# Kernel optimization log

Measured on AMD Instinct MI355X. Metric: run time of the kernel, lower is better.

The kernel has to match this reference:

```python
import jax, jax.numpy as jnp
import numpy as np

I, H, L, O = 11, 33, 3, 18

def lstm_layer(x_tbi, W_ih, W_hh, b_ih, b_hh):
    # x_tbi: [T, B, in]; W_ih: [4H, in]; W_hh: [4H, H]
    T, B = x_tbi.shape[0], x_tbi.shape[1]
    # precompute input contribution for all timesteps (one big GEMM)
    xg = jnp.einsum('tbi,gi->tbg', x_tbi, W_ih) + b_ih + b_hh  # [T, B, 4H]
    h0 = jnp.zeros((B, H), x_tbi.dtype)
    c0 = jnp.zeros((B, H), x_tbi.dtype)

    def step(carry, xg_t):
        h, c = carry
        gates = xg_t + h @ W_hh.T                      # [B, 4H]
        i, f, g, o = jnp.split(gates, 4, axis=-1)      # PyTorch gate order i,f,g,o
        i = jax.nn.sigmoid(i)
        f = jax.nn.sigmoid(f)
        g = jnp.tanh(g)
        o = jax.nn.sigmoid(o)
        c = f * c + i * g
        h = o * jnp.tanh(c)
        return (h, c), h

    (hT, cT), ys = jax.lax.scan(step, (h0, c0), xg)
    return ys, hT, cT  # ys: [T, B, H]


def setup_inputs() -> dict:
    key = jax.random.key(0)
    ks = jax.random.split(key, 20)
    B, T = 512, 2048
    s = 1.0 / np.sqrt(H)
    d = {'x': jax.random.normal(ks[0], (B, T, I), jnp.float32)}
    in_sizes = [I, H, H]
    for l in range(L):
        d[f'W_ih{l}'] = jax.random.uniform(ks[1 + 4 * l], (4 * H, in_sizes[l]), jnp.float32, -s, s)
        d[f'W_hh{l}'] = jax.random.uniform(ks[2 + 4 * l], (4 * H, H), jnp.float32, -s, s)
        d[f'b_ih{l}'] = jax.random.uniform(ks[3 + 4 * l], (4 * H,), jnp.float32, -s, s)
        d[f'b_hh{l}'] = jax.random.uniform(ks[4 + 4 * l], (4 * H,), jnp.float32, -s, s)
    d['W1'] = jax.random.normal(ks[13], (4 * O, H), jnp.float32) * 0.05
    d['b1'] = jnp.zeros((4 * O,), jnp.float32)
    d['W2'] = jax.random.normal(ks[14], (O, 4 * O), jnp.float32) * 0.05
    d['b2'] = jnp.zeros((O,), jnp.float32)
    return d


def reference(x, W_ih0, W_hh0, b_ih0, b_hh0, W_ih1, W_hh1, b_ih1, b_hh1,
              W_ih2, W_hh2, b_ih2, b_hh2, W1, b1, W2, b2):
    # x: [B, T, I] (batch_first) -> time-major for scan
    xt = jnp.transpose(x, (1, 0, 2))  # [T, B, I]
    params = [(W_ih0, W_hh0, b_ih0, b_hh0),
              (W_ih1, W_hh1, b_ih1, b_hh1),
              (W_ih2, W_hh2, b_ih2, b_hh2)]
    hiddens = []
    cur = xt
    for (Wi, Wh, bi, bh) in params:
        cur, hT, _ = lstm_layer(cur, Wi, Wh, bi, bh)
        hiddens.append(hT)
    hidden = jnp.stack(hiddens, axis=0)  # [L, B, H] (final hidden state per layer)
    # MLP head (dropout inactive at inference); torch nn.GELU default = exact erf
    h1 = jax.nn.gelu(hidden @ W1.T + b1, approximate=False)
    out = h1 @ W2.T + b2  # [L, B, O]
    return out, hidden
```

## Files before the change

### kernel.cpp

```cpp
#include <hip/hip_runtime.h>
#include <math.h>

#define TT 2048
#define BB 512
#define II 11
#define HH 33
#define NL 3
#define OO 18
#define HSLOT 48

typedef _Float16 h4 __attribute__((ext_vector_type(4)));
typedef _Float16 h8 __attribute__((ext_vector_type(8)));

__device__ __forceinline__ float sigm_f(float x) {
    float e = __expf(-x);
    return __builtin_amdgcn_rcpf(1.0f + e);
}
__device__ __forceinline__ float tanh_f(float x) {
    float e = __expf(2.0f * x);
    return 1.0f - 2.0f * __builtin_amdgcn_rcpf(e + 1.0f);
}

__device__ __forceinline__ float dpp_xor1(float v) {
    return __builtin_bit_cast(float,
        __builtin_amdgcn_update_dpp(0, __builtin_bit_cast(int, v), 0xB1, 0xF, 0xF, true));
}

__device__ __forceinline__ h8 gldh8(const float* p, int k0, int rem) {
    h8 v;
    #pragma unroll
    for (int i = 0; i < 8; ++i) v[i] = (_Float16)((k0 + i < rem) ? p[k0 + i] : 0.0f);
    return v;
}
__device__ __forceinline__ h4 gldh4(const float* p, int k0, int rem) {
    h4 v;
    #pragma unroll
    for (int i = 0; i < 4; ++i) v[i] = (_Float16)((k0 + i < rem) ? p[k0 + i] : 0.0f);
    return v;
}

#define D8(a, v, w) do { \
    a = __builtin_amdgcn_fdot2((v).s01, (w).s01, a, false); \
    a = __builtin_amdgcn_fdot2((v).s23, (w).s23, a, false); \
    a = __builtin_amdgcn_fdot2((v).s45, (w).s45, a, false); \
    a = __builtin_amdgcn_fdot2((v).s67, (w).s67, a, false); } while (0)
#define D4(a, v, w) do { \
    a = __builtin_amdgcn_fdot2((v).s01, (w).s01, a, false); \
    a = __builtin_amdgcn_fdot2((v).s23, (w).s23, a, false); } while (0)

__global__ __launch_bounds__(256, 2) void lstm_pipeline_kernel(
    const float* __restrict__ x,
    const float* __restrict__ Wih0, const float* __restrict__ Whh0,
    const float* __restrict__ bih0, const float* __restrict__ bhh0,
    const float* __restrict__ Wih1, const float* __restrict__ Whh1,
    const float* __restrict__ bih1, const float* __restrict__ bhh1,
    const float* __restrict__ Wih2, const float* __restrict__ Whh2,
    const float* __restrict__ bih2, const float* __restrict__ bhh2,
    float* __restrict__ hidden_out)
{
    __shared__ __align__(16) _Float16 buf[2][NL + 1][HSLOT];

    const int tid = threadIdx.x;
    const int bg  = blockIdx.x;

    for (int i = tid; i < 2 * (NL + 1) * HSLOT; i += 256)
        ((_Float16*)buf)[i] = (_Float16)0.0f;

    const bool comp = (tid < 198);
    const int  u    = tid >> 1;
    const int  p    = tid & 1;
    const int  l    = (u < 33) ? 0 : (u < 66) ? 1 : 2;
    const int  j    = u - 33 * l;

    const int  pi   = tid - 198;
    const bool pref = (pi >= 0) && (pi < II);
    const float* xrow = x + (size_t)bg * TT * II + (pref ? pi : 0);

    h8 z8 = {0,0,0,0,0,0,0,0};
    h4 z4 = {0,0,0,0};
    h8 w0a=z8,w0b=z8,w0c=z8,w0d=z8; h4 w0t=z4;
    h8 w1a=z8,w1b=z8,w1c=z8,w1d=z8; h4 w1t=z4;
    h8 w2a=z8,w2b=z8,w2c=z8,w2d=z8; h4 w2t=z4;
    h8 w3a=z8,w3b=z8,w3c=z8,w3d=z8; h4 w3t=z4;
    float b0 = 0.0f, b1 = 0.0f, b2 = 0.0f, b3 = 0.0f;

    if (comp) {
        const float* bip = (l == 0) ? bih0 : (l == 1) ? bih1 : bih2;
        const float* bhp = (l == 0) ? bhh0 : (l == 1) ? bhh1 : bhh2;
        if (p == 0) {
            b0 = bip[0 * HH + j] + bhp[0 * HH + j];
            b1 = bip[1 * HH + j] + bhp[1 * HH + j];
            b2 = bip[2 * HH + j] + bhp[2 * HH + j];
            b3 = bip[3 * HH + j] + bhp[3 * HH + j];
        }
        const float* Wsrc = p ? ((l == 0) ? Whh0 : (l == 1) ? Whh1 : Whh2)
                              : ((l == 0) ? Wih0 : (l == 1) ? Wih1 : Wih2);
        const int kin = (p || l != 0) ? HH : II;
        const float* r0 = Wsrc + (0 * HH + j) * kin;
        const float* r1 = Wsrc + (1 * HH + j) * kin;
        const float* r2 = Wsrc + (2 * HH + j) * kin;
        const float* r3 = Wsrc + (3 * HH + j) * kin;
        w0a = gldh8(r0, 0, kin); w0b = gldh8(r0, 8, kin);
        w0c = gldh8(r0, 16, kin); w0d = gldh8(r0, 24, kin); w0t = gldh4(r0, 32, kin);
        w1a = gldh8(r1, 0, kin); w1b = gldh8(r1, 8, kin);
        w1c = gldh8(r1, 16, kin); w1d = gldh8(r1, 24, kin); w1t = gldh4(r1, 32, kin);
        w2a = gldh8(r2, 0, kin); w2b = gldh8(r2, 8, kin);
        w2c = gldh8(r2, 16, kin); w2d = gldh8(r2, 24, kin); w2t = gldh4(r2, 32, kin);
        w3a = gldh8(r3, 0, kin); w3b = gldh8(r3, 8, kin);
        w3c = gldh8(r3, 16, kin); w3d = gldh8(r3, 24, kin); w3t = gldh4(r3, 32, kin);
    }

    __syncthreads();
    float v_next = 0.0f, v_next2 = 0.0f;
    if (pref) {
        buf[0][0][pi] = (_Float16)xrow[0];
        v_next  = xrow[II];
        v_next2 = xrow[2 * II];
    }
    __syncthreads();

    float c = 0.0f;
    const int   vsel = p ? (l + 1) : l;
    const float mA   = 1.0f + (float)p;
    const float cAc  = -(float)p;
    const bool  wrh  = comp && (p == 0);

    const _Float16* rd[2]  = { &buf[0][vsel][0], &buf[1][vsel][0] };
    _Float16*       wrp[2] = { &buf[0][l + 1][j], &buf[1][l + 1][j] };
    _Float16*       pxp[2] = { &buf[0][0][pi], &buf[1][0][pi] };

    auto step = [&](int s, int rp, bool check, bool out, bool xload, bool xstore)
        __attribute__((always_inline)) {
        const int wp = rp ^ 1;
        if (pref) {
            if (xstore) *pxp[wp] = (_Float16)v_next;
            v_next = v_next2;
            if (xload) v_next2 = xrow[(size_t)(s + 3) * II];
        }
        const bool active = check ? (comp && (s >= l) && (s - l < TT)) : comp;
        if (active) {
            const _Float16* V16 = rd[rp];
            const h8* V = (const h8*)V16;
            const h8 v0 = V[0], v1 = V[1], v2 = V[2], v3 = V[3];
            const h4 vt = *(const h4*)(V16 + 32);

            float a0 = b0, a1 = b1, a2 = b2, a3 = b3;
            D8(a0, v0, w0a); D8(a1, v0, w1a); D8(a2, v0, w2a); D8(a3, v0, w3a);
            D8(a0, v1, w0b); D8(a1, v1, w1b); D8(a2, v1, w2b); D8(a3, v1, w3b);
            D8(a0, v2, w0c); D8(a1, v2, w1c); D8(a2, v2, w2c); D8(a3, v2, w3c);
            D8(a0, v3, w0d); D8(a1, v3, w1d); D8(a2, v3, w2d); D8(a3, v3, w3d);
            D4(a0, vt, w0t); D4(a1, vt, w1t); D4(a2, vt, w2t); D4(a3, vt, w3t);

            a0 += dpp_xor1(a0); a1 += dpp_xor1(a1);
            a2 += dpp_xor1(a2); a3 += dpp_xor1(a3);

            const float aA = p ? a2 : a0;
            const float aB = p ? a3 : a1;
            const float acta = __builtin_fmaf(mA, sigm_f(mA * aA), cAc);
            const float actb = sigm_f(aB);
            const float xa = dpp_xor1(acta);
            const float xb = dpp_xor1(actb);
            const float ig = p ? xa : acta;
            const float gg = p ? acta : xa;
            const float fg = p ? xb : actb;
            const float og = p ? actb : xb;

            c = __builtin_fmaf(fg, c, ig * gg);
            const float hnew = og * tanh_f(c);

            if (wrh) {
                *wrp[wp] = (_Float16)hnew;
                if (out && (s - l == TT - 1))
                    hidden_out[((size_t)l * BB + bg) * HH + j] = hnew;
            }
        }
        __syncthreads();
    };

    step(0, 0, true, false, true, true);
    step(1, 1, true, false, true, true);
    for (int s = 2; s < TT - 4; s += 2) {
        step(s,     0, false, false, true, true);
        step(s + 1, 1, false, false, true, true);
    }
    step(TT - 4, 0, false, false, true,  true);
    step(TT - 3, 1, false, false, false, true);
    step(TT - 2, 0, false, false, false, true);
    step(TT - 1, 1, false, true,  false, false);
    step(TT,     0, true,  true,  false, false);
    step(TT + 1, 1, true,  true,  false, false);
}

__global__ void mlp_head_kernel(const float* __restrict__ hidden,
                                const float* __restrict__ W1, const float* __restrict__ b1,
                                const float* __restrict__ W2, const float* __restrict__ b2,
                                float* __restrict__ out)
{
    const int row = blockIdx.x * blockDim.x + threadIdx.x;
    if (row >= NL * BB) return;

    float hv[HH];
    #pragma unroll
    for (int k = 0; k < HH; ++k) hv[k] = hidden[row * HH + k];

    float h1[4 * OO];
    #pragma unroll
    for (int m = 0; m < 4 * OO; ++m) {
        float a = b1[m];
        #pragma unroll
        for (int k = 0; k < HH; ++k) a += hv[k] * W1[m * HH + k];
        h1[m] = 0.5f * a * (1.0f + erff(a * 0.70710678118654752f));
    }
    #pragma unroll
    for (int o = 0; o < OO; ++o) {
        float a = b2[o];
        #pragma unroll
        for (int m = 0; m < 4 * OO; ++m) a += h1[m] * W2[o * (4 * OO) + m];
        out[row * OO + o] = a;
    }
}

extern "C" void kernel_launch(void* const* d_in, const int* in_sizes, int n_in,
                              void* d_out, int out_size, void* d_ws, size_t ws_size,
                              hipStream_t stream) {
    const float* x    = (const float*)d_in[0];
    const float* Wih0 = (const float*)d_in[1];
    const float* Whh0 = (const float*)d_in[2];
    const float* bih0 = (const float*)d_in[3];
    const float* bhh0 = (const float*)d_in[4];
    const float* Wih1 = (const float*)d_in[5];
    const float* Whh1 = (const float*)d_in[6];
    const float* bih1 = (const float*)d_in[7];
    const float* bhh1 = (const float*)d_in[8];
    const float* Wih2 = (const float*)d_in[9];
    const float* Whh2 = (const float*)d_in[10];
    const float* bih2 = (const float*)d_in[11];
    const float* bhh2 = (const float*)d_in[12];
    const float* W1   = (const float*)d_in[13];
    const float* b1   = (const float*)d_in[14];
    const float* W2   = (const float*)d_in[15];
    const float* b2   = (const float*)d_in[16];

    float* out    = (float*)d_out;
    float* hidden = out + NL * BB * OO;

    lstm_pipeline_kernel<<<BB, 256, 0, stream>>>(
        x, Wih0, Whh0, bih0, bhh0, Wih1, Whh1, bih1, bhh1,
        Wih2, Whh2, bih2, bhh2, hidden);

    mlp_head_kernel<<<(NL * BB + 255) / 256, 256, 0, stream>>>(
        hidden, W1, b1, W2, b2, out);
}
```

Before: 1.190 ms.

## Use packed fp16 FMA accumulation for gate dot products and fuse MLP head

Replaces the fp32-accumulating fdot2 chains with packed half-precision FMAs into two h2 accumulators per gate, reduced across lanes in fp16 and then converted to fp32 with the bias. This halves the dependent chain length and uses packed math to shorten the per-timestep recurrent critical path. It also folds the MLP head into the LSTM kernel's epilogue using shared memory, removing a second launch. Accumulating 33-term dot products in fp16 reduces accuracy and may breach tolerance over 2048 recurrent steps.

Result: slower. 1.249 ms (+4.9%).

```diff
diff --git a/kernel.cpp b/kernel.cpp
--- a/kernel.cpp
+++ b/kernel.cpp
@@ -9,6 +9,7 @@
 #define OO 18
 #define HSLOT 48
 
+typedef _Float16 h2 __attribute__((ext_vector_type(2)));
 typedef _Float16 h4 __attribute__((ext_vector_type(4)));
 typedef _Float16 h8 __attribute__((ext_vector_type(8)));
 
@@ -23,6 +24,10 @@
 
 __device__ __forceinline__ float dpp_xor1(float v) {
     return __builtin_bit_cast(float,
+        __builtin_amdgcn_update_dpp(0, __builtin_bit_cast(int, v), 0xB1, 0xF, 0xF, true));
+}
+__device__ __forceinline__ h2 dpp_xor1_h2(h2 v) {
+    return __builtin_bit_cast(h2,
         __builtin_amdgcn_update_dpp(0, __builtin_bit_cast(int, v), 0xB1, 0xF, 0xF, true));
 }
 
@@ -39,14 +44,12 @@
     return v;
 }
 
-#define D8(a, v, w) do { \
-    a = __builtin_amdgcn_fdot2((v).s01, (w).s01, a, false); \
-    a = __builtin_amdgcn_fdot2((v).s23, (w).s23, a, false); \
-    a = __builtin_amdgcn_fdot2((v).s45, (w).s45, a, false); \
-    a = __builtin_amdgcn_fdot2((v).s67, (w).s67, a, false); } while (0)
-#define D4(a, v, w) do { \
-    a = __builtin_amdgcn_fdot2((v).s01, (w).s01, a, false); \
-    a = __builtin_amdgcn_fdot2((v).s23, (w).s23, a, false); } while (0)
+#define PF(acc, vv, ww) acc = __builtin_elementwise_fma((vv), (ww), (acc))
+#define PK8(A, B, v, w) do { \
+    PF(A, (v).s01, (w).s01); PF(B, (v).s23, (w).s23); \
+    PF(A, (v).s45, (w).s45); PF(B, (v).s67, (w).s67); } while (0)
+#define PK4(A, B, v, w) do { \
+    PF(A, (v).s01, (w).s01); PF(B, (v).s23, (w).s23); } while (0)
 
 __global__ __launch_bounds__(256, 2) void lstm_pipeline_kernel(
     const float* __restrict__ x,
@@ -56,9 +59,14 @@
     const float* __restrict__ bih1, const float* __restrict__ bhh1,
     const float* __restrict__ Wih2, const float* __restrict__ Whh2,
     const float* __restrict__ bih2, const float* __restrict__ bhh2,
-    float* __restrict__ hidden_out)
+    const float* __restrict__ W1, const float* __restrict__ b1,
+    const float* __restrict__ W2, const float* __restrict__ b2,
+    float* __restrict__ hidden_out,
+    float* __restrict__ outp)
 {
     __shared__ __align__(16) _Float16 buf[2][NL + 1][HSLOT];
+    __shared__ float hfin[NL][HH];
+    __shared__ float h1s[NL][4 * OO];
 
     const int tid = threadIdx.x;
     const int bg  = blockIdx.x;
@@ -82,17 +90,16 @@
     h8 w1a=z8,w1b=z8,w1c=z8,w1d=z8; h4 w1t=z4;
     h8 w2a=z8,w2b=z8,w2c=z8,w2d=z8; h4 w2t=z4;
     h8 w3a=z8,w3b=z8,w3c=z8,w3d=z8; h4 w3t=z4;
-    float b0 = 0.0f, b1 = 0.0f, b2 = 0.0f, b3 = 0.0f;
+    float b0 = 0.0f, b1v = 0.0f, b2v = 0.0f, b3v = 0.0f;
 
     if (comp) {
         const float* bip = (l == 0) ? bih0 : (l == 1) ? bih1 : bih2;
         const float* bhp = (l == 0) ? bhh0 : (l == 1) ? bhh1 : bhh2;
-        if (p == 0) {
-            b0 = bip[0 * HH + j] + bhp[0 * HH + j];
-            b1 = bip[1 * HH + j] + bhp[1 * HH + j];
-            b2 = bip[2 * HH + j] + bhp[2 * HH + j];
-            b3 = bip[3 * HH + j] + bhp[3 * HH + j];
-        }
+        b0  = bip[0 * HH + j] + bhp[0 * HH + j];
+        b1v = bip[1 * HH + j] + bhp[1 * HH + j];
+        b2v = bip[2 * HH + j] + bhp[2 * HH + j];
+        b3v = bip[3 * HH + j] + bhp[3 * HH + j];
+
         const float* Wsrc = p ? ((l == 0) ? Whh0 : (l == 1) ? Whh1 : Whh2)
                               : ((l == 0) ? Wih0 : (l == 1) ? Wih1 : Wih2);
         const int kin = (p || l != 0) ? HH : II;
@@ -144,15 +151,28 @@
             const h8 v0 = V[0], v1 = V[1], v2 = V[2], v3 = V[3];
             const h4 vt = *(const h4*)(V16 + 32);
 
-            float a0 = b0, a1 = b1, a2 = b2, a3 = b3;
-            D8(a0, v0, w0a); D8(a1, v0, w1a); D8(a2, v0, w2a); D8(a3, v0, w3a);
-            D8(a0, v1, w0b); D8(a1, v1, w1b); D8(a2, v1, w2b); D8(a3, v1, w3b);
-            D8(a0, v2, w0c); D8(a1, v2, w1c); D8(a2, v2, w2c); D8(a3, v2, w3c);
-            D8(a0, v3, w0d); D8(a1, v3, w1d); D8(a2, v3, w2d); D8(a3, v3, w3d);
-            D4(a0, vt, w0t); D4(a1, vt, w1t); D4(a2, vt, w2t); D4(a3, vt, w3t);
-
-            a0 += dpp_xor1(a0); a1 += dpp_xor1(a1);
-            a2 += dpp_xor1(a2); a3 += dpp_xor1(a3);
+            h2 z2 = {(_Float16)0.0f, (_Float16)0.0f};
+            h2 A0 = z2, B0 = z2, A1 = z2, B1 = z2;
+            h2 A2 = z2, B2 = z2, A3 = z2, B3 = z2;
+            PK8(A0, B0, v0, w0a); PK8(A1, B1, v0, w1a);
+            PK8(A2, B2, v0, w2a); PK8(A3, B3, v0, w3a);
+            PK8(A0, B0, v1, w0b); PK8(A1, B1, v1, w1b);
+            PK8(A2, B2, v1, w2b); PK8(A3, B3, v1, w3b);
+            PK8(A0, B0, v2, w0c); PK8(A1, B1, v2, w1c);
+            PK8(A2, B2, v2, w2c); PK8(A3, B3, v2, w3c);
+            PK8(A0, B0, v3, w0d); PK8(A1, B1, v3, w1d);
+            PK8(A2, B2, v3, w2d); PK8(A3, B3, v3, w3d);
+            PK4(A0, B0, vt, w0t); PK4(A1, B1, vt, w1t);
+            PK4(A2, B2, vt, w2t); PK4(A3, B3, vt, w3t);
+
+            h2 t0 = A0 + B0, t1 = A1 + B1, t2 = A2 + B2, t3 = A3 + B3;
+            t0 += dpp_xor1_h2(t0); t1 += dpp_xor1_h2(t1);
+            t2 += dpp_xor1_h2(t2); t3 += dpp_xor1_h2(t3);
+
+            const float a0 = b0  + ((float)t0.x + (float)t0.y);
+            const float a1 = b1v + ((float)t1.x + (float)t1.y);
+            const float a2 = b2v + ((float)t2.x + (float)t2.y);
+            const float a3 = b3v + ((float)t3.x + (float)t3.y);
 
             const float aA = p ? a2 : a0;
             const float aB = p ? a3 : a1;
@@ -170,8 +190,10 @@
 
             if (wrh) {
                 *wrp[wp] = (_Float16)hnew;
-                if (out && (s - l == TT - 1))
+                if (out && (s - l == TT - 1)) {
                     hidden_out[((size_t)l * BB + bg) * HH + j] = hnew;
+                    hfin[l][j] = hnew;
+                }
             }
         }
         __syncthreads();
@@ -189,34 +211,21 @@
     step(TT - 1, 1, false, true,  false, false);
     step(TT,     0, true,  true,  false, false);
     step(TT + 1, 1, true,  true,  false, false);
-}
-
-__global__ void mlp_head_kernel(const float* __restrict__ hidden,
-                                const float* __restrict__ W1, const float* __restrict__ b1,
-                                const float* __restrict__ W2, const float* __restrict__ b2,
-                                float* __restrict__ out)
-{
-    const int row = blockIdx.x * blockDim.x + threadIdx.x;
-    if (row >= NL * BB) return;
-
-    float hv[HH];
-    #pragma unroll
-    for (int k = 0; k < HH; ++k) hv[k] = hidden[row * HH + k];
-
-    float h1[4 * OO];
-    #pragma unroll
-    for (int m = 0; m < 4 * OO; ++m) {
+
+    if (tid < NL * 4 * OO) {
+        const int ml = tid / (4 * OO), m = tid % (4 * OO);
         float a = b1[m];
         #pragma unroll
-        for (int k = 0; k < HH; ++k) a += hv[k] * W1[m * HH + k];
-        h1[m] = 0.5f * a * (1.0f + erff(a * 0.70710678118654752f));
-    }
-    #pragma unroll
-    for (int o = 0; o < OO; ++o) {
+        for (int k = 0; k < HH; ++k) a += hfin[ml][k] * W1[m * HH + k];
+        h1s[ml][m] = 0.5f * a * (1.0f + erff(a * 0.70710678118654752f));
+    }
+    __syncthreads();
+    if (tid < NL * OO) {
+        const int ol = tid / OO, o = tid % OO;
         float a = b2[o];
         #pragma unroll
-        for (int m = 0; m < 4 * OO; ++m) a += h1[m] * W2[o * (4 * OO) + m];
-        out[row * OO + o] = a;
+        for (int m = 0; m < 4 * OO; ++m) a += h1s[ol][m] * W2[o * (4 * OO) + m];
+        outp[((size_t)ol * BB + bg) * OO + o] = a;
     }
 }
 
@@ -246,8 +255,5 @@
 
     lstm_pipeline_kernel<<<BB, 256, 0, stream>>>(
         x, Wih0, Whh0, bih0, bhh0, Wih1, Whh1, bih1, bhh1,
-        Wih2, Whh2, bih2, bhh2, hidden);
-
-    mlp_head_kernel<<<(NL * BB + 255) / 256, 256, 0, stream>>>(
-        hidden, W1, b1, W2, b2, out);
-}
+        Wih2, Whh2, bih2, bhh2, W1, b1, W2, b2, hidden, out);
+}
```

## Use one thread per hidden unit instead of paired threads per unit

Applied to the files above, without the earlier changes.

Each hidden unit is now computed by a single thread that holds both the input and recurrent weight rows in registers. This removes the DPP cross-lane reductions and gate exchanges, and shrinks the block from 256 to 128 threads (two waves instead of four), which cuts barrier cost. The price is twice the serial dot-product work per thread on the recurrent critical path and roughly double the weight registers per thread. It also drops the padded tail from 4 to 2 halves.

After: 1.150 ms. 3.4% less time.

```diff
diff --git a/kernel.cpp b/kernel.cpp
--- a/kernel.cpp
+++ b/kernel.cpp
@@ -9,7 +9,7 @@
 #define OO 18
 #define HSLOT 48
 
-typedef _Float16 h4 __attribute__((ext_vector_type(4)));
+typedef _Float16 h2 __attribute__((ext_vector_type(2)));
 typedef _Float16 h8 __attribute__((ext_vector_type(8)));
 
 __device__ __forceinline__ float sigm_f(float x) {
@@ -21,21 +21,16 @@
     return 1.0f - 2.0f * __builtin_amdgcn_rcpf(e + 1.0f);
 }
 
-__device__ __forceinline__ float dpp_xor1(float v) {
-    return __builtin_bit_cast(float,
-        __builtin_amdgcn_update_dpp(0, __builtin_bit_cast(int, v), 0xB1, 0xF, 0xF, true));
-}
-
 __device__ __forceinline__ h8 gldh8(const float* p, int k0, int rem) {
     h8 v;
     #pragma unroll
     for (int i = 0; i < 8; ++i) v[i] = (_Float16)((k0 + i < rem) ? p[k0 + i] : 0.0f);
     return v;
 }
-__device__ __forceinline__ h4 gldh4(const float* p, int k0, int rem) {
-    h4 v;
-    #pragma unroll
-    for (int i = 0; i < 4; ++i) v[i] = (_Float16)((k0 + i < rem) ? p[k0 + i] : 0.0f);
+__device__ __forceinline__ h2 gldh2(const float* p, int k0, int rem) {
+    h2 v;
+    v.x = (_Float16)((k0 + 0 < rem) ? p[k0 + 0] : 0.0f);
+    v.y = (_Float16)((k0 + 1 < rem) ? p[k0 + 1] : 0.0f);
     return v;
 }
 
@@ -44,11 +39,9 @@
     a = __builtin_amdgcn_fdot2((v).s23, (w).s23, a, false); \
     a = __builtin_amdgcn_fdot2((v).s45, (w).s45, a, false); \
     a = __builtin_amdgcn_fdot2((v).s67, (w).s67, a, false); } while (0)
-#define D4(a, v, w) do { \
-    a = __builtin_amdgcn_fdot2((v).s01, (w).s01, a, false); \
-    a = __builtin_amdgcn_fdot2((v).s23, (w).s23, a, false); } while (0)
-
-__global__ __launch_bounds__(256, 2) void lstm_pipeline_kernel(
+#define D1(a, v, w) a = __builtin_amdgcn_fdot2((v), (w), a, false)
+
+__global__ __launch_bounds__(128, 1) void lstm_pipeline_kernel(
     const float* __restrict__ x,
     const float* __restrict__ Wih0, const float* __restrict__ Whh0,
     const float* __restrict__ bih0, const float* __restrict__ bhh0,
@@ -63,51 +56,57 @@
     const int tid = threadIdx.x;
     const int bg  = blockIdx.x;
 
-    for (int i = tid; i < 2 * (NL + 1) * HSLOT; i += 256)
+    for (int i = tid; i < 2 * (NL + 1) * HSLOT; i += 128)
         ((_Float16*)buf)[i] = (_Float16)0.0f;
 
-    const bool comp = (tid < 198);
-    const int  u    = tid >> 1;
-    const int  p    = tid & 1;
+    const bool comp = (tid < 99);
+    const int  u    = tid;
     const int  l    = (u < 33) ? 0 : (u < 66) ? 1 : 2;
     const int  j    = u - 33 * l;
 
-    const int  pi   = tid - 198;
+    const int  pi   = tid - 99;
     const bool pref = (pi >= 0) && (pi < II);
     const float* xrow = x + (size_t)bg * TT * II + (pref ? pi : 0);
 
     h8 z8 = {0,0,0,0,0,0,0,0};
-    h4 z4 = {0,0,0,0};
-    h8 w0a=z8,w0b=z8,w0c=z8,w0d=z8; h4 w0t=z4;
-    h8 w1a=z8,w1b=z8,w1c=z8,w1d=z8; h4 w1t=z4;
-    h8 w2a=z8,w2b=z8,w2c=z8,w2d=z8; h4 w2t=z4;
-    h8 w3a=z8,w3b=z8,w3c=z8,w3d=z8; h4 w3t=z4;
+    h2 z2 = {(_Float16)0.0f, (_Float16)0.0f};
+    h8 x00=z8,x01=z8,x02=z8,x03=z8; h2 x0t=z2;
+    h8 x10=z8,x11=z8,x12=z8,x13=z8; h2 x1t=z2;
+    h8 x20=z8,x21=z8,x22=z8,x23=z8; h2 x2t=z2;
+    h8 x30=z8,x31=z8,x32=z8,x33=z8; h2 x3t=z2;
+    h8 h00=z8,h01=z8,h02=z8,h03=z8; h2 h0t=z2;
+    h8 h10=z8,h11=z8,h12=z8,h13=z8; h2 h1t=z2;
+    h8 h20=z8,h21=z8,h22=z8,h23=z8; h2 h2t=z2;
+    h8 h30=z8,h31=z8,h32=z8,h33=z8; h2 h3t=z2;
     float b0 = 0.0f, b1 = 0.0f, b2 = 0.0f, b3 = 0.0f;
 
     if (comp) {
         const float* bip = (l == 0) ? bih0 : (l == 1) ? bih1 : bih2;
         const float* bhp = (l == 0) ? bhh0 : (l == 1) ? bhh1 : bhh2;
-        if (p == 0) {
-            b0 = bip[0 * HH + j] + bhp[0 * HH + j];
-            b1 = bip[1 * HH + j] + bhp[1 * HH + j];
-            b2 = bip[2 * HH + j] + bhp[2 * HH + j];
-            b3 = bip[3 * HH + j] + bhp[3 * HH + j];
-        }
-        const float* Wsrc = p ? ((l == 0) ? Whh0 : (l == 1) ? Whh1 : Whh2)
-                              : ((l == 0) ? Wih0 : (l == 1) ? Wih1 : Wih2);
-        const int kin = (p || l != 0) ? HH : II;
-        const float* r0 = Wsrc + (0 * HH + j) * kin;
-        const float* r1 = Wsrc + (1 * HH + j) * kin;
-        const float* r2 = Wsrc + (2 * HH + j) * kin;
-        const float* r3 = Wsrc + (3 * HH + j) * kin;
-        w0a = gldh8(r0, 0, kin); w0b = gldh8(r0, 8, kin);
-        w0c = gldh8(r0, 16, kin); w0d = gldh8(r0, 24, kin); w0t = gldh4(r0, 32, kin);
-        w1a = gldh8(r1, 0, kin); w1b = gldh8(r1, 8, kin);
-        w1c = gldh8(r1, 16, kin); w1d = gldh8(r1, 24, kin); w1t = gldh4(r1, 32, kin);
-        w2a = gldh8(r2, 0, kin); w2b = gldh8(r2, 8, kin);
-        w2c = gldh8(r2, 16, kin); w2d = gldh8(r2, 24, kin); w2t = gldh4(r2, 32, kin);
-        w3a = gldh8(r3, 0, kin); w3b = gldh8(r3, 8, kin);
-        w3c = gldh8(r3, 16, kin); w3d = gldh8(r3, 24, kin); w3t = gldh4(r3, 32, kin);
+        b0 = bip[0 * HH + j] + bhp[0 * HH + j];
+        b1 = bip[1 * HH + j] + bhp[1 * HH + j];
+        b2 = bip[2 * HH + j] + bhp[2 * HH + j];
+        b3 = bip[3 * HH + j] + bhp[3 * HH + j];
+
+        const float* Wi = (l == 0) ? Wih0 : (l == 1) ? Wih1 : Wih2;
+        const float* Wh = (l == 0) ? Whh0 : (l == 1) ? Whh1 : Whh2;
+        const int kin = (l == 0) ? II : HH;
+        const float* r0 = Wi + (0 * HH + j) * kin;
+        const float* r1 = Wi + (1 * HH + j) * kin;
+        const float* r2 = Wi + (2 * HH + j) * kin;
+        const float* r3 = Wi + (3 * HH + j) * kin;
+        x00=gldh8(r0,0,kin); x01=gldh8(r0,8,kin); x02=gldh8(r0,16,kin); x03=gldh8(r0,24,kin); x0t=gldh2(r0,32,kin);
+        x10=gldh8(r1,0,kin); x11=gldh8(r1,8,kin); x12=gldh8(r1,16,kin); x13=gldh8(r1,24,kin); x1t=gldh2(r1,32,kin);
+        x20=gldh8(r2,0,kin); x21=gldh8(r2,8,kin); x22=gldh8(r2,16,kin); x23=gldh8(r2,24,kin); x2t=gldh2(r2,32,kin);
+        x30=gldh8(r3,0,kin); x31=gldh8(r3,8,kin); x32=gldh8(r3,16,kin); x33=gldh8(r3,24,kin); x3t=gldh2(r3,32,kin);
+        const float* s0 = Wh + (0 * HH + j) * HH;
+        const float* s1 = Wh + (1 * HH + j) * HH;
+        const float* s2 = Wh + (2 * HH + j) * HH;
+        const float* s3 = Wh + (3 * HH + j) * HH;
+        h00=gldh8(s0,0,HH); h01=gldh8(s0,8,HH); h02=gldh8(s0,16,HH); h03=gldh8(s0,24,HH); h0t=gldh2(s0,32,HH);
+        h10=gldh8(s1,0,HH); h11=gldh8(s1,8,HH); h12=gldh8(s1,16,HH); h13=gldh8(s1,24,HH); h1t=gldh2(s1,32,HH);
+        h20=gldh8(s2,0,HH); h21=gldh8(s2,8,HH); h22=gldh8(s2,16,HH); h23=gldh8(s2,24,HH); h2t=gldh2(s2,32,HH);
+        h30=gldh8(s3,0,HH); h31=gldh8(s3,8,HH); h32=gldh8(s3,16,HH); h33=gldh8(s3,24,HH); h3t=gldh2(s3,32,HH);
     }
 
     __syncthreads();
@@ -120,14 +119,11 @@
     __syncthreads();
 
     float c = 0.0f;
-    const int   vsel = p ? (l + 1) : l;
-    const float mA   = 1.0f + (float)p;
-    const float cAc  = -(float)p;
-    const bool  wrh  = comp && (p == 0);
-
-    const _Float16* rd[2]  = { &buf[0][vsel][0], &buf[1][vsel][0] };
-    _Float16*       wrp[2] = { &buf[0][l + 1][j], &buf[1][l + 1][j] };
-    _Float16*       pxp[2] = { &buf[0][0][pi], &buf[1][0][pi] };
+
+    const _Float16* rin[2]  = { &buf[0][l][0],     &buf[1][l][0] };
+    const _Float16* rown[2] = { &buf[0][l + 1][0], &buf[1][l + 1][0] };
+    _Float16*       wrp[2]  = { &buf[0][l + 1][j], &buf[1][l + 1][j] };
+    _Float16*       pxp[2]  = { &buf[0][0][pi],    &buf[1][0][pi] };
 
     auto step = [&](int s, int rp, bool check, bool out, bool xload, bool xstore)
         __attribute__((always_inline)) {
@@ -139,40 +135,35 @@
         }
         const bool active = check ? (comp && (s >= l) && (s - l < TT)) : comp;
         if (active) {
-            const _Float16* V16 = rd[rp];
-            const h8* V = (const h8*)V16;
-            const h8 v0 = V[0], v1 = V[1], v2 = V[2], v3 = V[3];
-            const h4 vt = *(const h4*)(V16 + 32);
+            const h8* VI = (const h8*)rin[rp];
+            const h8 vi0 = VI[0], vi1 = VI[1], vi2 = VI[2], vi3 = VI[3];
+            const h2 vit = *(const h2*)(rin[rp] + 32);
+            const h8* VO = (const h8*)rown[rp];
+            const h8 vo0 = VO[0], vo1 = VO[1], vo2 = VO[2], vo3 = VO[3];
+            const h2 vot = *(const h2*)(rown[rp] + 32);
 
             float a0 = b0, a1 = b1, a2 = b2, a3 = b3;
-            D8(a0, v0, w0a); D8(a1, v0, w1a); D8(a2, v0, w2a); D8(a3, v0, w3a);
-            D8(a0, v1, w0b); D8(a1, v1, w1b); D8(a2, v1, w2b); D8(a3, v1, w3b);
-            D8(a0, v2, w0c); D8(a1, v2, w1c); D8(a2, v2, w2c); D8(a3, v2, w3c);
-            D8(a0, v3, w0d); D8(a1, v3, w1d); D8(a2, v3, w2d); D8(a3, v3, w3d);
-            D4(a0, vt, w0t); D4(a1, vt, w1t); D4(a2, vt, w2t); D4(a3, vt, w3t);
-
-            a0 += dpp_xor1(a0); a1 += dpp_xor1(a1);
-            a2 += dpp_xor1(a2); a3 += dpp_xor1(a3);
-
-            const float aA = p ? a2 : a0;
-            const float aB = p ? a3 : a1;
-            const float acta = __builtin_fmaf(mA, sigm_f(mA * aA), cAc);
-            const float actb = sigm_f(aB);
-            const float xa = dpp_xor1(acta);
-            const float xb = dpp_xor1(actb);
-            const float ig = p ? xa : acta;
-            const float gg = p ? acta : xa;
-            const float fg = p ? xb : actb;
-            const float og = p ? actb : xb;
-
+            D8(a0, vi0, x00); D8(a1, vi0, x10); D8(a2, vi0, x20); D8(a3, vi0, x30);
+            D8(a0, vi1, x01); D8(a1, vi1, x11); D8(a2, vi1, x21); D8(a3, vi1, x31);
+            D8(a0, vi2, x02); D8(a1, vi2, x12); D8(a2, vi2, x22); D8(a3, vi2, x32);
+            D8(a0, vi3, x03); D8(a1, vi3, x13); D8(a2, vi3, x23); D8(a3, vi3, x33);
+            D1(a0, vit, x0t); D1(a1, vit, x1t); D1(a2, vit, x2t); D1(a3, vit, x3t);
+            D8(a0, vo0, h00); D8(a1, vo0, h10); D8(a2, vo0, h20); D8(a3, vo0, h30);
+            D8(a0, vo1, h01); D8(a1, vo1, h11); D8(a2, vo1, h21); D8(a3, vo1, h31);
+            D8(a0, vo2, h02); D8(a1, vo2, h12); D8(a2, vo2, h22); D8(a3, vo2, h32);
+            D8(a0, vo3, h03); D8(a1, vo3, h13); D8(a2, vo3, h23); D8(a3, vo3, h33);
+            D1(a0, vot, h0t); D1(a1, vot, h1t); D1(a2, vot, h2t); D1(a3, vot, h3t);
+
+            const float ig = sigm_f(a0);
+            const float fg = sigm_f(a1);
+            const float gg = tanh_f(a2);
+            const float og = sigm_f(a3);
             c = __builtin_fmaf(fg, c, ig * gg);
             const float hnew = og * tanh_f(c);
 
-            if (wrh) {
-                *wrp[wp] = (_Float16)hnew;
-                if (out && (s - l == TT - 1))
-                    hidden_out[((size_t)l * BB + bg) * HH + j] = hnew;
-            }
+            *wrp[wp] = (_Float16)hnew;
+            if (out && (s - l == TT - 1))
+                hidden_out[((size_t)l * BB + bg) * HH + j] = hnew;
         }
         __syncthreads();
     };
@@ -244,7 +235,7 @@
     float* out    = (float*)d_out;
     float* hidden = out + NL * BB * OO;
 
-    lstm_pipeline_kernel<<<BB, 256, 0, stream>>>(
+    lstm_pipeline_kernel<<<BB, 128, 0, stream>>>(
         x, Wih0, Whh0, bih0, bhh0, Wih1, Whh1, bih1, bhh1,
         Wih2, Whh2, bih2, bhh2, hidden);
 
```
